# Optimization experiments

Measured on AMD Instinct MI355X. Metric: run time of the kernel, lower is better.

Reference implementation:

```python
import jax, jax.numpy as jnp
import numpy as np

B, S, D = 1, 2048, 2048
H, G, HD = 32, 8, 64
EPS = 1e-6
ROPE_BASE = 10000.0


def rms_norm(x, g):
    # torch RMSNorm computed in fp32 then cast back (PytorchRMSNorm wrapper)
    xf = x.astype(jnp.float32)
    y = xf * jax.lax.rsqrt(jnp.mean(xf * xf, axis=-1, keepdims=True) + EPS) * g.astype(jnp.float32)
    return y.astype(x.dtype)


def rotate_half(x):
    x1, x2 = jnp.split(x, 2, axis=-1)
    return jnp.concatenate([-x2, x1], axis=-1)


def apply_rope(x, cos, sin):
    # x: (b, h, s, hd); cos/sin: (s, hd)
    return x * cos[None, None] + rotate_half(x) * sin[None, None]


def setup_inputs() -> dict:
    key = jax.random.key(0)
    ks = jax.random.split(key, 8)
    x = jax.random.normal(ks[0], (B, S, D), dtype=jnp.float32)
    wq = jax.random.normal(ks[1], (H * HD, D), dtype=jnp.float32) * (D ** -0.5)
    wk = jax.random.normal(ks[2], (G * HD, D), dtype=jnp.float32) * (D ** -0.5)
    wv = jax.random.normal(ks[3], (G * HD, D), dtype=jnp.float32) * (D ** -0.5)
    wo = jax.random.normal(ks[4], (D, H * HD), dtype=jnp.float32) * (D ** -0.5)
    qg = jnp.ones((HD,), dtype=jnp.float32)
    kg = jnp.ones((HD,), dtype=jnp.float32)
    # RoPE tables (HF-style: duplicated half-dim frequencies)
    inv_freq = 1.0 / (ROPE_BASE ** (jnp.arange(0, HD, 2, dtype=jnp.float32) / HD))
    ang = jnp.arange(S, dtype=jnp.float32)[:, None] * inv_freq[None, :]  # (S, HD/2)
    emb = jnp.concatenate([ang, ang], axis=-1)  # (S, HD)
    cos = jnp.cos(emb)
    sin = jnp.sin(emb)
    # causal mask: True = future (upper-right triangle)
    mask = jnp.triu(jnp.ones((S, S), dtype=bool), k=1)
    return {"x": x, "mask": mask, "cos": cos, "sin": sin,
            "wq": wq, "wk": wk, "wv": wv, "wo": wo, "qg": qg, "kg": kg}


def reference(x, mask, cos, sin, wq, wk, wv, wo, qg, kg):
    b, s, _ = x.shape
    rep = H // G
    q = (x @ wq.T).reshape(b, s, H, HD).transpose(0, 2, 1, 3)   # (b,H,s,hd)
    k = (x @ wk.T).reshape(b, s, G, HD).transpose(0, 2, 1, 3)   # (b,G,s,hd)
    v = (x @ wv.T).reshape(b, s, G, HD).transpose(0, 2, 1, 3)
    q = rms_norm(q, qg)
    k = rms_norm(k, kg)
    q = apply_rope(q, cos[:s], sin[:s])
    k = apply_rope(k, cos[:s], sin[:s])
    k = jnp.repeat(k, rep, axis=1)  # (b,H,s,hd) GQA expansion
    v = jnp.repeat(v, rep, axis=1)
    scores = jnp.einsum('bhqd,bhkd->bhqk', q, k) * (HD ** -0.5)
    neg = jnp.finfo(scores.dtype).min / 2
    scores = jnp.where(mask[None, None, :s, :s], neg, scores)
    w = jax.nn.softmax(scores, axis=-1)
    ctx = jnp.einsum('bhqk,bhkd->bhqd', w, v)
    ctx = ctx.transpose(0, 2, 1, 3).reshape(b, s, H * HD)
    return ctx @ wo.T
```

## Files before the change

### kernel.cpp

```cpp
#include <hip/hip_runtime.h>
#include <stdint.h>

#define SEQ    2048
#define DMODEL 2048
#define NHEAD  32
#define NKV    8
#define HDIM   64
#define NQKV   3072

typedef __bf16 bf16x8 __attribute__((ext_vector_type(8)));
typedef float  f32x4  __attribute__((ext_vector_type(4)));

#define SCALE2 0.180336880f
#define THR2   12.0f

__device__ __forceinline__ ushort bf(float f){
  __bf16 h = (__bf16)f;
  return __builtin_bit_cast(unsigned short, h);
}
__device__ __forceinline__ float b2f(ushort v){
  union { uint32_t u; float f; } a; a.u = ((uint32_t)v) << 16; return a.f;
}

__device__ __forceinline__ void gl_lds16(const void* g, void* l){
  __builtin_amdgcn_global_load_lds(
      (const __attribute__((address_space(1))) uint32_t*)g,
      (__attribute__((address_space(3))) uint32_t*)l, 16, 0, 0);
}

__global__ __launch_bounds__(256) void k_cvt_all(const float* __restrict__ x,
                                                 const float* __restrict__ wq,
                                                 const float* __restrict__ wk,
                                                 const float* __restrict__ wv,
                                                 const float* __restrict__ wo,
                                                 ushort* __restrict__ xb,
                                                 ushort* __restrict__ wcat,
                                                 ushort* __restrict__ wob){
  int i = blockIdx.x * 256 + threadIdx.x;
  const float* src; ushort* dst; int s4; int d4;
  if (i < 1048576)      { src = x;  dst = xb;   s4 = i;           d4 = s4; }
  else if (i < 2097152) { src = wq; dst = wcat; s4 = i - 1048576; d4 = s4; }
  else if (i < 2359296) { src = wk; dst = wcat; s4 = i - 2097152; d4 = s4 + 1048576; }
  else if (i < 2621440) { src = wv; dst = wcat; s4 = i - 2359296; d4 = s4 + 1310720; }
  else                  { src = wo; dst = wob;  s4 = i - 2621440; d4 = s4; }
  float4 v = reinterpret_cast<const float4*>(src)[s4];
  ushort4 o;
  o.x = bf(v.x); o.y = bf(v.y); o.z = bf(v.z); o.w = bf(v.w);
  reinterpret_cast<ushort4*>(dst)[d4] = o;
}

__global__ __launch_bounds__(256) void k_gemm_bt(const ushort* __restrict__ A,
                                                 const ushort* __restrict__ B,
                                                 float* __restrict__ C,
                                                 int M, int N, int K){
  __shared__ ushort As[2][128*64];
  __shared__ ushort Bs[2][128*64];
  const int tid = threadIdx.x, lane = tid & 63, wid = tid >> 6;
  const int bm = blockIdx.y * 128, bn = blockIdx.x * 128;
  const int wr = wid >> 1, wc = wid & 1;
  const int l15 = lane & 15, u = lane >> 4;

  const int srow = wid*32 + (lane >> 3);
  const int scol = ((lane & 7) ^ (lane >> 3)) * 8;
  const ushort* Abase = A + (size_t)(bm + srow) * K + scol;
  const ushort* Bbase = B + (size_t)(bn + srow) * K + scol;

  auto STAGE = [&](int buf, int k0){
#pragma unroll
    for (int c = 0; c < 4; c++){
      gl_lds16(Abase + k0 + (size_t)c*8*K, &As[buf][(wid*32 + c*8)*64]);
      gl_lds16(Bbase + k0 + (size_t)c*8*K, &Bs[buf][(wid*32 + c*8)*64]);
    }
  };

  f32x4 acc[4][4] = {};
  const int NT = K >> 6;

  STAGE(0, 0);
  __syncthreads();

  for (int t = 0; t < NT; t++){
    const int cur = t & 1;
    if (t + 1 < NT) STAGE(cur ^ 1, (t + 1) << 6);

#pragma unroll
    for (int kc = 0; kc < 2; kc++){
      bf16x8 af[4], bfr[4];
#pragma unroll
      for (int m = 0; m < 4; m++){
        int row = wr*64 + m*16 + l15;
        af[m] = *reinterpret_cast<const bf16x8*>(&As[cur][row*64 + (((kc*4+u) ^ (row&7))*8)]);
      }
#pragma unroll
      for (int n = 0; n < 4; n++){
        int row = wc*64 + n*16 + l15;
        bfr[n] = *reinterpret_cast<const bf16x8*>(&Bs[cur][row*64 + (((kc*4+u) ^ (row&7))*8)]);
      }
      __builtin_amdgcn_s_setprio(1);
#pragma unroll
      for (int m = 0; m < 4; m++)
#pragma unroll
        for (int n = 0; n < 4; n++)
          acc[m][n] = __builtin_amdgcn_mfma_f32_16x16x32_bf16(af[m], bfr[n], acc[m][n], 0, 0, 0);
      __builtin_amdgcn_s_setprio(0);
    }

    __syncthreads();
  }

#pragma unroll
  for (int m = 0; m < 4; m++)
#pragma unroll
    for (int n = 0; n < 4; n++)
#pragma unroll
      for (int j = 0; j < 4; j++){
        int row = bm + wr*64 + m*16 + u*4 + j;
        int col = bn + wc*64 + n*16 + l15;
        C[(size_t)row * N + col] = acc[m][n][j];
      }
}

__global__ __launch_bounds__(256) void k_gemm_btc(const ushort* __restrict__ A,
                                                  const ushort* __restrict__ B,
                                                  ushort* __restrict__ C,
                                                  int M, int N, int K){
  __shared__ ushort As[2][128*64];
  __shared__ ushort Bs[2][128*64];
  const int tid = threadIdx.x, lane = tid & 63, wid = tid >> 6;
  const int bm = blockIdx.y * 128, bn = blockIdx.x * 128;
  const int wr = wid >> 1, wc = wid & 1;
  const int l15 = lane & 15, u = lane >> 4;

  const int srow = wid*32 + (lane >> 3);
  const int scol = ((lane & 7) ^ (lane >> 3)) * 8;
  const ushort* Abase = A + (size_t)(bm + srow) * K + scol;
  const ushort* Bbase = B + (size_t)(bn + srow) * K + scol;

  auto STAGE = [&](int buf, int k0){
#pragma unroll
    for (int c = 0; c < 4; c++){
      gl_lds16(Abase + k0 + (size_t)c*8*K, &As[buf][(wid*32 + c*8)*64]);
      gl_lds16(Bbase + k0 + (size_t)c*8*K, &Bs[buf][(wid*32 + c*8)*64]);
    }
  };

  f32x4 acc[4][4] = {};
  const int NT = K >> 6;

  STAGE(0, 0);
  __syncthreads();

  for (int t = 0; t < NT; t++){
    const int cur = t & 1;
    if (t + 1 < NT) STAGE(cur ^ 1, (t + 1) << 6);

#pragma unroll
    for (int kc = 0; kc < 2; kc++){
      bf16x8 af[4], bfr[4];
#pragma unroll
      for (int m = 0; m < 4; m++){
        int row = wr*64 + m*16 + l15;
        af[m] = *reinterpret_cast<const bf16x8*>(&As[cur][row*64 + (((kc*4+u) ^ (row&7))*8)]);
      }
#pragma unroll
      for (int n = 0; n < 4; n++){
        int row = wc*64 + n*16 + l15;
        bfr[n] = *reinterpret_cast<const bf16x8*>(&Bs[cur][row*64 + (((kc*4+u) ^ (row&7))*8)]);
      }
      __builtin_amdgcn_s_setprio(1);
#pragma unroll
      for (int m = 0; m < 4; m++)
#pragma unroll
        for (int n = 0; n < 4; n++)
          acc[m][n] = __builtin_amdgcn_mfma_f32_16x16x32_bf16(af[m], bfr[n], acc[m][n], 0, 0, 0);
      __builtin_amdgcn_s_setprio(0);
    }

    __syncthreads();
  }

#pragma unroll
  for (int m = 0; m < 4; m++)
#pragma unroll
    for (int n = 0; n < 4; n++)
#pragma unroll
      for (int j = 0; j < 4; j++){
        int row = bm + wr*64 + m*16 + u*4 + j;
        int col = bn + wc*64 + n*16 + l15;
        C[(size_t)row * N + col] = bf(acc[m][n][j]);
      }
}

__global__ __launch_bounds__(256) void k_normrope(const ushort* __restrict__ qkvc,
                                                  const float* __restrict__ cosp,
                                                  const float* __restrict__ sinp,
                                                  const float* __restrict__ qg,
                                                  const float* __restrict__ kg,
                                                  ushort* __restrict__ qb,
                                                  ushort* __restrict__ kb){
  const int s = blockIdx.x;
  const int tid = threadIdx.x, lane = tid & 63, wid = tid >> 6;
  const ushort* row = qkvc + (size_t)s * NQKV;
  const float cs = cosp[s*HDIM + lane];
  const float sn = sinp[s*HDIM + lane];

  for (int hidx = wid; hidx < 40; hidx += 4){
    const bool isq = hidx < 32;
    const int col = isq ? hidx*64 : 2048 + (hidx-32)*64;
    float x = b2f(row[col + lane]);
    float ss = x * x;
#pragma unroll
    for (int m = 1; m < 64; m <<= 1) ss += __shfl_xor(ss, m);
    float r = rsqrtf(ss * (1.0f/64.0f) + 1e-6f);
    float y = x * r * (isq ? qg : kg)[lane];
    float p = __shfl_xor(y, 32);
    float out = y * cs + (lane < 32 ? -p : p) * sn;
    if (isq) qb[(size_t)s*2048 + hidx*64 + lane] = bf(out * SCALE2);
    else     kb[(size_t)s*512 + (hidx-32)*64 + lane] = bf(out);
  }
}

__global__ __launch_bounds__(256) void k_vtrans(const ushort* __restrict__ qkvc,
                                                ushort* __restrict__ vtb){
  __shared__ ushort tile[64][68];
  const int g = blockIdx.x >> 5, st = blockIdx.x & 31;
  const int tid = threadIdx.x;
#pragma unroll
  for (int i = 0; i < 4; i++){
    int idx = i*256 + tid;
    int r = idx >> 4, c4 = idx & 15;
    ushort4 v = *reinterpret_cast<const ushort4*>(
        qkvc + (size_t)(st*64 + r)*NQKV + 2560 + g*64 + c4*4);
    tile[c4*4+0][r] = v.x;
    tile[c4*4+1][r] = v.y;
    tile[c4*4+2][r] = v.z;
    tile[c4*4+3][r] = v.w;
  }
  __syncthreads();
#pragma unroll
  for (int i = 0; i < 4; i++){
    int idx = i*256 + tid;
    int d = idx >> 4, s4 = idx & 15;
    int pos4 = (s4 >> 3)*32 + (s4 & 3)*8 + ((s4 >> 2) & 1)*4;
    ushort4 o = *reinterpret_cast<const ushort4*>(&tile[d][s4*4]);
    *reinterpret_cast<ushort4*>(vtb + (size_t)(g*64 + d)*SEQ + st*64 + pos4) = o;
  }
}

__global__ __launch_bounds__(256) void k_attn(const ushort* __restrict__ qbuf,
                                              const ushort* __restrict__ kbuf,
                                              const ushort* __restrict__ vtb,
                                              ushort* __restrict__ ctx){
  __shared__ ushort Kd[3][64*64];
  __shared__ ushort Vd[3][64*64];

  const int bx = blockIdx.x;
  const int c  = bx & 255, sl = bx >> 8;
  const int cg = c >> 5,  h  = c & 31;
  const int qt = (sl == 0) ? 31 - cg : (sl == 1) ? 16 + cg
               : (sl == 2) ? 15 - cg : cg;
  const int g = h >> 2;
  const int tid = threadIdx.x, lane = tid & 63, wid = tid >> 6;
  const int l15 = lane & 15, u = lane >> 4;
  const int q0 = qt*64 + wid*16;
  const int tmax = qt;

  bf16x8 qf[2];
#pragma unroll
  for (int kc = 0; kc < 2; kc++)
    qf[kc] = *reinterpret_cast<const bf16x8*>(
        qbuf + (size_t)(q0 + l15)*2048 + h*64 + kc*32 + u*8);

  f32x4 o[4] = {};
  float mrun = -1e30f;
  float lrun = 0.f;

  int koff[8], voff[8];
#pragma unroll
  for (int kb = 0; kb < 4; kb++)
#pragma unroll
    for (int kc = 0; kc < 2; kc++){
      int keyl = kb*16 + l15;
      koff[kb*2+kc] = (keyl*64 + (((kc*4+u) ^ (keyl&7))*8)) * 2;
    }
#pragma unroll
  for (int kc = 0; kc < 2; kc++)
#pragma unroll
    for (int d0 = 0; d0 < 4; d0++){
      int vrow = d0*16 + l15;
      voff[kc*4+d0] = (vrow*64 + (((kc*4+u) ^ (vrow&7))*8)) * 2;
    }

  const int srow = wid*16 + (lane >> 3);
  const int scol = ((lane & 7) ^ (lane >> 3)) * 8;
  const ushort* ksrc0 = kbuf + (size_t)srow*512 + g*64 + scol;
  const ushort* vsrc0 = vtb  + (size_t)(g*64 + srow)*SEQ + scol;

  auto STAGE = [&](int buf, int t){
    const ushort* ks = ksrc0 + (size_t)t*64*512;
    gl_lds16(ks,         &Kd[buf][wid*1024]);
    gl_lds16(ks + 8*512, &Kd[buf][wid*1024 + 512]);
    const ushort* vs = vsrc0 + t*64;
    gl_lds16(vs,          &Vd[buf][wid*1024]);
    gl_lds16(vs + 8*SEQ,  &Vd[buf][wid*1024 + 512]);
  };

  STAGE(0, 0);
  if (tmax >= 1) STAGE(1, 1);

  for (int t = 0; t <= tmax; t++){
    const int cur = t % 3;
    if (t < tmax) asm volatile("s_waitcnt vmcnt(4)" ::: "memory");
    else          asm volatile("s_waitcnt vmcnt(0)" ::: "memory");
    __builtin_amdgcn_s_barrier();
    __builtin_amdgcn_sched_barrier(0);
    if (t + 2 <= tmax) STAGE((t + 2) % 3, t + 2);

    const char* KB = (const char*)Kd + cur*8192;
    const char* VB = (const char*)Vd + cur*8192;
    const bool full = (t*64 + 63) <= q0;

    f32x4 st[4];
    __builtin_amdgcn_s_setprio(1);
#pragma unroll
    for (int kb = 0; kb < 4; kb++){
      const int key0 = t*64 + kb*16;
      if (key0 <= q0 + 15){
        bf16x8 kf0 = *reinterpret_cast<const bf16x8*>(KB + koff[kb*2]);
        bf16x8 kf1 = *reinterpret_cast<const bf16x8*>(KB + koff[kb*2+1]);
        f32x4 a = {};
        a = __builtin_amdgcn_mfma_f32_16x16x32_bf16(kf0, qf[0], a, 0, 0, 0);
        a = __builtin_amdgcn_mfma_f32_16x16x32_bf16(kf1, qf[1], a, 0, 0, 0);
        st[kb] = a;
      } else {
        st[kb] = (f32x4){-1e30f, -1e30f, -1e30f, -1e30f};
      }
    }
    __builtin_amdgcn_s_setprio(0);
    if (!full){
      const int keyb = t*64 + u*4;
      const int qr = q0 + l15;
#pragma unroll
      for (int kb = 0; kb < 4; kb++)
#pragma unroll
        for (int j = 0; j < 4; j++)
          st[kb][j] = (keyb + kb*16 + j > qr) ? -1e30f : st[kb][j];
    }

    {
      f32x4 mx = st[0];
#pragma unroll
      for (int kb = 1; kb < 4; kb++)
#pragma unroll
        for (int j = 0; j < 4; j++) mx[j] = fmaxf(mx[j], st[kb][j]);
      float tml = fmaxf(fmaxf(mx[0], mx[1]), fmaxf(mx[2], mx[3]));
      if (__any(tml > mrun + THR2)){
        float tm = fmaxf(tml, __shfl_xor(tml, 16));
        tm = fmaxf(tm, __shfl_xor(tm, 32));
        float mn = fmaxf(mrun, tm);
        float al = exp2f(mrun - mn);
        mrun = mn;
        lrun *= al;
#pragma unroll
        for (int d0 = 0; d0 < 4; d0++)
#pragma unroll
          for (int j = 0; j < 4; j++) o[d0][j] *= al;
      }
#pragma unroll
      for (int kb = 0; kb < 4; kb++)
#pragma unroll
        for (int j = 0; j < 4; j++){
          float p = exp2f(st[kb][j] - mrun);
          st[kb][j] = p;
          lrun += p;
        }
    }

    __builtin_amdgcn_s_setprio(1);
#pragma unroll
    for (int kc = 0; kc < 2; kc++){
      union { uint32_t w[4]; bf16x8 v; } pb;
      asm("v_cvt_pk_bf16_f32 %0, %1, %2" : "=v"(pb.w[0]) : "v"(st[2*kc  ][0]), "v"(st[2*kc  ][1]));
      asm("v_cvt_pk_bf16_f32 %0, %1, %2" : "=v"(pb.w[1]) : "v"(st[2*kc  ][2]), "v"(st[2*kc  ][3]));
      asm("v_cvt_pk_bf16_f32 %0, %1, %2" : "=v"(pb.w[2]) : "v"(st[2*kc+1][0]), "v"(st[2*kc+1][1]));
      asm("v_cvt_pk_bf16_f32 %0, %1, %2" : "=v"(pb.w[3]) : "v"(st[2*kc+1][2]), "v"(st[2*kc+1][3]));
#pragma unroll
      for (int d0 = 0; d0 < 4; d0++){
        bf16x8 vb8 = *reinterpret_cast<const bf16x8*>(VB + voff[kc*4+d0]);
        o[d0] = __builtin_amdgcn_mfma_f32_16x16x32_bf16(vb8, pb.v, o[d0], 0, 0, 0);
      }
    }
    __builtin_amdgcn_s_setprio(0);
  }

  {
    float lt = lrun + __shfl_xor(lrun, 16);
    lt += __shfl_xor(lt, 32);
    float inv = 1.0f / lt;
#pragma unroll
    for (int d0 = 0; d0 < 4; d0++){
      ushort4 w;
      w.x = bf(o[d0][0] * inv); w.y = bf(o[d0][1] * inv);
      w.z = bf(o[d0][2] * inv); w.w = bf(o[d0][3] * inv);
      *reinterpret_cast<ushort4*>(
          &ctx[(size_t)(q0 + l15)*2048 + h*64 + d0*16 + u*4]) = w;
    }
  }
}

extern "C" void kernel_launch(void* const* d_in, const int* in_sizes, int n_in,
                              void* d_out, int out_size, void* d_ws, size_t ws_size,
                              hipStream_t stream){
  const float* x    = (const float*)d_in[0];
  const float* cosp = (const float*)d_in[2];
  const float* sinp = (const float*)d_in[3];
  const float* wq   = (const float*)d_in[4];
  const float* wk   = (const float*)d_in[5];
  const float* wv   = (const float*)d_in[6];
  const float* wo   = (const float*)d_in[7];
  const float* qg   = (const float*)d_in[8];
  const float* kg   = (const float*)d_in[9];
  float* out = (float*)d_out;

  char* ws = (char*)d_ws;
  ushort* xb   = (ushort*)(ws);
  ushort* wcat = (ushort*)(ws + 8388608);
  ushort* wob  = (ushort*)(ws + 20971520);
  ushort* qkvc = (ushort*)(ws + 29360128);
  ushort* qb   = (ushort*)(ws + 41943040);
  ushort* kb   = (ushort*)(ws + 50331648);
  ushort* vtb  = (ushort*)(ws + 52428800);
  ushort* ctxb = (ushort*)(ws + 54525952);

  k_cvt_all<<<14336, 256, 0, stream>>>(x, wq, wk, wv, wo, xb, wcat, wob);
  k_gemm_btc<<<dim3(24, 16), 256, 0, stream>>>(xb, wcat, qkvc, 2048, 3072, 2048);
  k_normrope<<<2048, 256, 0, stream>>>(qkvc, cosp, sinp, qg, kg, qb, kb);
  k_vtrans<<<256, 256, 0, stream>>>(qkvc, vtb);
  k_attn<<<1024, 256, 0, stream>>>(qb, kb, vtb, ctxb);
  k_gemm_bt<<<dim3(16, 16), 256, 0, stream>>>(ctxb, wob, out, 2048, 2048, 2048);
}
```

Baseline: 151.1 us.

## Process two GQA query heads per attention block to share K/V tiles

Each attention block now handles two query heads that share a KV group, so every staged K/V tile in LDS and every K/V fragment load feeds two sets of MFMAs. The grid is halved and the query-tile scheduling is reworked into two slices of causal tiles paired long/short. This cuts K/V global and LDS traffic per unit of work, at the cost of more registers per thread (doubled accumulators and softmax state) and fewer blocks, which may lower occupancy and worsen load balance.

```diff
diff --git a/kernel.cpp b/kernel.cpp
--- a/kernel.cpp
+++ b/kernel.cpp
@@ -255,25 +255,28 @@
   __shared__ ushort Vd[3][64*64];
 
   const int bx = blockIdx.x;
-  const int c  = bx & 255, sl = bx >> 8;
-  const int cg = c >> 5,  h  = c & 31;
-  const int qt = (sl == 0) ? 31 - cg : (sl == 1) ? 16 + cg
-               : (sl == 2) ? 15 - cg : cg;
-  const int g = h >> 2;
+  const int sl  = bx >> 8, idx = bx & 255;
+  const int qtr = idx >> 3;
+  const int hp  = (idx & 7) | (sl << 3);
+  const int qt  = sl ? qtr : 31 - qtr;
+  const int g   = hp >> 1;
+  const int h0  = g*4 + (hp & 1)*2;
   const int tid = threadIdx.x, lane = tid & 63, wid = tid >> 6;
   const int l15 = lane & 15, u = lane >> 4;
   const int q0 = qt*64 + wid*16;
   const int tmax = qt;
 
-  bf16x8 qf[2];
-#pragma unroll
-  for (int kc = 0; kc < 2; kc++)
-    qf[kc] = *reinterpret_cast<const bf16x8*>(
-        qbuf + (size_t)(q0 + l15)*2048 + h*64 + kc*32 + u*8);
-
-  f32x4 o[4] = {};
-  float mrun = -1e30f;
-  float lrun = 0.f;
+  bf16x8 qf[2][2];
+#pragma unroll
+  for (int hh = 0; hh < 2; hh++)
+#pragma unroll
+    for (int kc = 0; kc < 2; kc++)
+      qf[hh][kc] = *reinterpret_cast<const bf16x8*>(
+          qbuf + (size_t)(q0 + l15)*2048 + (h0+hh)*64 + kc*32 + u*8);
+
+  f32x4 o[2][4] = {};
+  float mrun[2] = {-1e30f, -1e30f};
+  float lrun[2] = {0.f, 0.f};
 
   int koff[8], voff[8];
 #pragma unroll
@@ -320,7 +323,7 @@
     const char* VB = (const char*)Vd + cur*8192;
     const bool full = (t*64 + 63) <= q0;
 
-    f32x4 st[4];
+    f32x4 st[2][4];
     __builtin_amdgcn_s_setprio(1);
 #pragma unroll
     for (int kb = 0; kb < 4; kb++){
@@ -328,12 +331,17 @@
       if (key0 <= q0 + 15){
         bf16x8 kf0 = *reinterpret_cast<const bf16x8*>(KB + koff[kb*2]);
         bf16x8 kf1 = *reinterpret_cast<const bf16x8*>(KB + koff[kb*2+1]);
-        f32x4 a = {};
-        a = __builtin_amdgcn_mfma_f32_16x16x32_bf16(kf0, qf[0], a, 0, 0, 0);
-        a = __builtin_amdgcn_mfma_f32_16x16x32_bf16(kf1, qf[1], a, 0, 0, 0);
-        st[kb] = a;
+#pragma unroll
+        for (int hh = 0; hh < 2; hh++){
+          f32x4 a = {};
+          a = __builtin_amdgcn_mfma_f32_16x16x32_bf16(kf0, qf[hh][0], a, 0, 0, 0);
+          a = __builtin_amdgcn_mfma_f32_16x16x32_bf16(kf1, qf[hh][1], a, 0, 0, 0);
+          st[hh][kb] = a;
+        }
       } else {
-        st[kb] = (f32x4){-1e30f, -1e30f, -1e30f, -1e30f};
+#pragma unroll
+        for (int hh = 0; hh < 2; hh++)
+          st[hh][kb] = (f32x4){-1e30f, -1e30f, -1e30f, -1e30f};
       }
     }
     __builtin_amdgcn_s_setprio(0);
@@ -343,67 +351,77 @@
 #pragma unroll
       for (int kb = 0; kb < 4; kb++)
 #pragma unroll
-        for (int j = 0; j < 4; j++)
-          st[kb][j] = (keyb + kb*16 + j > qr) ? -1e30f : st[kb][j];
-    }
-
-    {
-      f32x4 mx = st[0];
+        for (int j = 0; j < 4; j++){
+          const bool msk = (keyb + kb*16 + j > qr);
+#pragma unroll
+          for (int hh = 0; hh < 2; hh++)
+            st[hh][kb][j] = msk ? -1e30f : st[hh][kb][j];
+        }
+    }
+
+#pragma unroll
+    for (int hh = 0; hh < 2; hh++){
+      f32x4 mx = st[hh][0];
 #pragma unroll
       for (int kb = 1; kb < 4; kb++)
 #pragma unroll
-        for (int j = 0; j < 4; j++) mx[j] = fmaxf(mx[j], st[kb][j]);
+        for (int j = 0; j < 4; j++) mx[j] = fmaxf(mx[j], st[hh][kb][j]);
       float tml = fmaxf(fmaxf(mx[0], mx[1]), fmaxf(mx[2], mx[3]));
-      if (__any(tml > mrun + THR2)){
+      if (__any(tml > mrun[hh] + THR2)){
         float tm = fmaxf(tml, __shfl_xor(tml, 16));
         tm = fmaxf(tm, __shfl_xor(tm, 32));
-        float mn = fmaxf(mrun, tm);
-        float al = exp2f(mrun - mn);
-        mrun = mn;
-        lrun *= al;
+        float mn = fmaxf(mrun[hh], tm);
+        float al = exp2f(mrun[hh] - mn);
+        mrun[hh] = mn;
+        lrun[hh] *= al;
 #pragma unroll
         for (int d0 = 0; d0 < 4; d0++)
 #pragma unroll
-          for (int j = 0; j < 4; j++) o[d0][j] *= al;
+          for (int j = 0; j < 4; j++) o[hh][d0][j] *= al;
       }
 #pragma unroll
       for (int kb = 0; kb < 4; kb++)
 #pragma unroll
         for (int j = 0; j < 4; j++){
-          float p = exp2f(st[kb][j] - mrun);
-          st[kb][j] = p;
-          lrun += p;
+          float p = exp2f(st[hh][kb][j] - mrun[hh]);
+          st[hh][kb][j] = p;
+          lrun[hh] += p;
         }
     }
 
     __builtin_amdgcn_s_setprio(1);
 #pragma unroll
     for (int kc = 0; kc < 2; kc++){
-      union { uint32_t w[4]; bf16x8 v; } pb;
-      asm("v_cvt_pk_bf16_f32 %0, %1, %2" : "=v"(pb.w[0]) : "v"(st[2*kc  ][0]), "v"(st[2*kc  ][1]));
-      asm("v_cvt_pk_bf16_f32 %0, %1, %2" : "=v"(pb.w[1]) : "v"(st[2*kc  ][2]), "v"(st[2*kc  ][3]));
-      asm("v_cvt_pk_bf16_f32 %0, %1, %2" : "=v"(pb.w[2]) : "v"(st[2*kc+1][0]), "v"(st[2*kc+1][1]));
-      asm("v_cvt_pk_bf16_f32 %0, %1, %2" : "=v"(pb.w[3]) : "v"(st[2*kc+1][2]), "v"(st[2*kc+1][3]));
+      union { uint32_t w[4]; bf16x8 v; } pb[2];
+#pragma unroll
+      for (int hh = 0; hh < 2; hh++){
+        asm("v_cvt_pk_bf16_f32 %0, %1, %2" : "=v"(pb[hh].w[0]) : "v"(st[hh][2*kc  ][0]), "v"(st[hh][2*kc  ][1]));
+        asm("v_cvt_pk_bf16_f32 %0, %1, %2" : "=v"(pb[hh].w[1]) : "v"(st[hh][2*kc  ][2]), "v"(st[hh][2*kc  ][3]));
+        asm("v_cvt_pk_bf16_f32 %0, %1, %2" : "=v"(pb[hh].w[2]) : "v"(st[hh][2*kc+1][0]), "v"(st[hh][2*kc+1][1]));
+        asm("v_cvt_pk_bf16_f32 %0, %1, %2" : "=v"(pb[hh].w[3]) : "v"(st[hh][2*kc+1][2]), "v"(st[hh][2*kc+1][3]));
+      }
 #pragma unroll
       for (int d0 = 0; d0 < 4; d0++){
         bf16x8 vb8 = *reinterpret_cast<const bf16x8*>(VB + voff[kc*4+d0]);
-        o[d0] = __builtin_amdgcn_mfma_f32_16x16x32_bf16(vb8, pb.v, o[d0], 0, 0, 0);
+        o[0][d0] = __builtin_amdgcn_mfma_f32_16x16x32_bf16(vb8, pb[0].v, o[0][d0], 0, 0, 0);
+        o[1][d0] = __builtin_amdgcn_mfma_f32_16x16x32_bf16(vb8, pb[1].v, o[1][d0], 0, 0, 0);
       }
     }
     __builtin_amdgcn_s_setprio(0);
   }
 
-  {
-    float lt = lrun + __shfl_xor(lrun, 16);
+#pragma unroll
+  for (int hh = 0; hh < 2; hh++){
+    float lt = lrun[hh] + __shfl_xor(lrun[hh], 16);
     lt += __shfl_xor(lt, 32);
     float inv = 1.0f / lt;
 #pragma unroll
     for (int d0 = 0; d0 < 4; d0++){
       ushort4 w;
-      w.x = bf(o[d0][0] * inv); w.y = bf(o[d0][1] * inv);
-      w.z = bf(o[d0][2] * inv); w.w = bf(o[d0][3] * inv);
+      w.x = bf(o[hh][d0][0] * inv); w.y = bf(o[hh][d0][1] * inv);
+      w.z = bf(o[hh][d0][2] * inv); w.w = bf(o[hh][d0][3] * inv);
       *reinterpret_cast<ushort4*>(
-          &ctx[(size_t)(q0 + l15)*2048 + h*64 + d0*16 + u*4]) = w;
+          &ctx[(size_t)(q0 + l15)*2048 + (h0+hh)*64 + d0*16 + u*4]) = w;
     }
   }
 }
@@ -436,6 +454,6 @@
   k_gemm_btc<<<dim3(24, 16), 256, 0, stream>>>(xb, wcat, qkvc, 2048, 3072, 2048);
   k_normrope<<<2048, 256, 0, stream>>>(qkvc, cosp, sinp, qg, kg, qb, kb);
   k_vtrans<<<256, 256, 0, stream>>>(qkvc, vtb);
-  k_attn<<<1024, 256, 0, stream>>>(qb, kb, vtb, ctxb);
+  k_attn<<<512, 256, 0, stream>>>(qb, kb, vtb, ctxb);
   k_gemm_bt<<<dim3(16, 16), 256, 0, stream>>>(ctxb, wob, out, 2048, 2048, 2048);
 }
```

Measured after the change: 167.7 us. 1.11x slower.
